# Optimization experiments

Hardware: AMD Instinct MI355X
Metric: run time of the kernel (lower is better)

## Reference

```python
import jax, jax.numpy as jnp
import numpy as np

N, E = 50000, 800000
IN, HID, OUT, L = 512, 64, 40, 16
ALPHA, LAMBDA = 0.1, 0.5


def setup_inputs() -> dict:
    key = jax.random.key(0)
    ks = jax.random.split(key, 8)
    features = jax.random.normal(ks[0], (N, IN), jnp.float32)
    src = jax.random.randint(ks[1], (E,), 0, N)
    dst = jax.random.randint(ks[2], (E,), 0, N)
    # fcs[0]: Linear(IN, HID); fcs[1]: Linear(HID, OUT)
    W_in = jax.random.normal(ks[3], (IN, HID), jnp.float32) / np.sqrt(IN)
    b_in = jnp.zeros((HID,), jnp.float32)
    W_out = jax.random.normal(ks[4], (HID, OUT), jnp.float32) / np.sqrt(HID)
    b_out = jnp.zeros((OUT,), jnp.float32)
    # per-layer GCN2Conv weights (project_initial_features=False -> weight1 & weight2) + bias
    W1 = jax.random.normal(ks[5], (L, HID, HID), jnp.float32) / np.sqrt(HID)
    W2 = jax.random.normal(ks[6], (L, HID, HID), jnp.float32) / np.sqrt(HID)
    b = jnp.zeros((L, HID), jnp.float32)
    return dict(features=features, W_in=W_in, b_in=b_in, W1=W1, W2=W2, b=b,
                W_out=W_out, b_out=b_out, src=src, dst=dst)


def reference(features, W_in, b_in, W1, W2, b, W_out, b_out, src, dst):
    ones = jnp.ones((E,), jnp.float32)
    deg_out = jax.ops.segment_sum(ones, src, num_segments=N)
    deg_in = jax.ops.segment_sum(ones, dst, num_segments=N)
    norm_src = jnp.maximum(deg_out, 1.0) ** -0.5  # [N]
    norm_dst = jnp.maximum(deg_in, 1.0) ** -0.5   # [N]
    betas = jnp.log(LAMBDA / jnp.arange(1, L + 1, dtype=jnp.float32) + 1.0)

    # inference: dropout is identity
    h0 = jax.nn.relu(features @ W_in + b_in)  # [N, HID]

    def layer(h, params):
        w1, w2, bias, beta = params
        # symmetric-normalized sparse propagation: D^-1/2 A D^-1/2 h
        hs = h * norm_src[:, None]
        agg = jax.ops.segment_sum(hs[src], dst, num_segments=N) * norm_dst[:, None]
        f = (1.0 - ALPHA) * agg   # smoothed part
        f0 = ALPHA * h0           # initial residual
        rst = (1.0 - beta) * f + beta * (f @ w1)
        rst = rst + (1.0 - beta) * f0 + beta * (f0 @ w2)
        rst = rst + bias
        return jax.nn.relu(rst), None

    h, _ = jax.lax.scan(layer, h0, (W1, W2, b, betas))
    logits = h @ W_out + b_out  # [N, OUT]
    return jax.nn.log_softmax(logits, axis=1)
```

## Files before the change

### kernel.cpp

```cpp
#include <hip/hip_runtime.h>
#include <math.h>

#define NN 50000
#define NE 800000
#define INF 512
#define HID 64
#define OUTF 40
#define NL 16

#define NBLK 256
#define EPB 3125
#define NBUK 196
#define SLEN (NBUK * NBLK)

#define TN 32
#define FP 72

using short8 = __attribute__((ext_vector_type(8))) short;
using f32x4v = __attribute__((ext_vector_type(4))) float;

__device__ __forceinline__ unsigned int f2bf(float f) {
    unsigned int u = __float_as_uint(f);
    return (u + 0x7fffu + ((u >> 16) & 1u)) >> 16;
}
__device__ __forceinline__ float bflo(unsigned int w) { return __uint_as_float(w << 16); }
__device__ __forceinline__ float bfhi(unsigned int w) { return __uint_as_float(w & 0xffff0000u); }
__device__ __forceinline__ float bfs(unsigned short u) { return __uint_as_float(((unsigned)u) << 16); }


__global__ __launch_bounds__(256) void k_cnt(const int* __restrict__ src, const int* __restrict__ dst,
                                             int* __restrict__ cnt2) {
    __shared__ int hD[NBUK];
    __shared__ int hS[NBUK];
    int t = threadIdx.x;
    int blk = blockIdx.x;
    if (t < NBUK) { hD[t] = 0; hS[t] = 0; }
    __syncthreads();
    int s0 = blk * EPB;
    for (int i = t; i < EPB; i += 256) {
        int e = s0 + i;
        atomicAdd(&hD[dst[e] >> 8], 1);
        atomicAdd(&hS[src[e] >> 8], 1);
    }
    __syncthreads();
    if (t < NBUK) {
        cnt2[t * NBLK + blk] = hD[t];
        cnt2[SLEN + t * NBLK + blk] = hS[t];
    }
}

__global__ __launch_bounds__(256) void gscanA(const int* __restrict__ in, int* __restrict__ incl,
                                              int* __restrict__ bsum, int len) {
    __shared__ int lds[256];
    int i = blockIdx.x * 256 + threadIdx.x;
    int v = (i < len) ? in[i] : 0;
    lds[threadIdx.x] = v;
    __syncthreads();
    for (int off = 1; off < 256; off <<= 1) {
        int t = (threadIdx.x >= off) ? lds[threadIdx.x - off] : 0;
        __syncthreads();
        lds[threadIdx.x] += t;
        __syncthreads();
    }
    if (i < len) incl[i] = lds[threadIdx.x];
    if (threadIdx.x == 255) bsum[blockIdx.x] = lds[255];
}

__global__ __launch_bounds__(512) void gscanB(int* __restrict__ bsum, int nb) {
    __shared__ int lds[512];
    int v = (threadIdx.x < nb) ? bsum[threadIdx.x] : 0;
    lds[threadIdx.x] = v;
    __syncthreads();
    for (int off = 1; off < 512; off <<= 1) {
        int t = (threadIdx.x >= off) ? lds[threadIdx.x - off] : 0;
        __syncthreads();
        lds[threadIdx.x] += t;
        __syncthreads();
    }
    if (threadIdx.x < nb) bsum[threadIdx.x] = lds[threadIdx.x] - v;
}

__global__ __launch_bounds__(256) void gscanC(const int* __restrict__ incl, const int* __restrict__ in,
                                              const int* __restrict__ bsum, int* __restrict__ off, int len) {
    int i = blockIdx.x * 256 + threadIdx.x;
    if (i < len) off[i] = incl[i] - in[i] + bsum[i >> 8] - ((i >= SLEN) ? NE : 0);
}

__global__ __launch_bounds__(256) void k_scat(const int* __restrict__ src, const int* __restrict__ dst,
                                              const int* __restrict__ offD, const int* __restrict__ offS,
                                              uint2* __restrict__ edst, int* __restrict__ esrc) {
    __shared__ int cD[NBUK];
    __shared__ int cS[NBUK];
    int t = threadIdx.x;
    int blk = blockIdx.x;
    if (t < NBUK) { cD[t] = 0; cS[t] = 0; }
    __syncthreads();
    int s0 = blk * EPB;
    for (int i = t; i < EPB; i += 256) {
        int e = s0 + i;
        int d = dst[e];
        int s = src[e];
        int bD = d >> 8;
        int r = atomicAdd(&cD[bD], 1);
        uint2 v;
        v.x = (unsigned)d;
        v.y = (unsigned)s;
        edst[offD[bD * NBLK + blk] + r] = v;
        int bS = s >> 8;
        int r2 = atomicAdd(&cS[bS], 1);
        esrc[offS[bS * NBLK + blk] + r2] = s;
    }
}

__global__ __launch_bounds__(256) void k_build(const uint2* __restrict__ edst, const int* __restrict__ esrc,
                                               const int* __restrict__ offD, const int* __restrict__ offS,
                                               float* __restrict__ nd, int* __restrict__ row_start,
                                               int* __restrict__ col, float* __restrict__ ns) {
    __shared__ int cnt[256];
    __shared__ int ex[256];
    __shared__ int cur[256];
    int t = threadIdx.x;
    if (blockIdx.x < NBUK) {
        int b = blockIdx.x;
        int base = offD[b * NBLK];
        int end = (b < NBUK - 1) ? offD[(b + 1) * NBLK] : NE;
        cnt[t] = 0;
        __syncthreads();
        for (int p = base + t; p < end; p += 256) {
            uint2 ed = edst[p];
            atomicAdd(&cnt[ed.x & 255], 1);
        }
        __syncthreads();
        int v = cnt[t];
        ex[t] = v;
        __syncthreads();
        for (int off = 1; off < 256; off <<= 1) {
            int tv = (t >= off) ? ex[t - off] : 0;
            __syncthreads();
            ex[t] += tv;
            __syncthreads();
        }
        int excl = ex[t] - v;
        cur[t] = excl;
        int node = b * 256 + t;
        if (node < NN) {
            nd[node] = 1.0f / sqrtf((float)max(v, 1));
            row_start[node] = base + excl;
        }
        __syncthreads();
        for (int p = base + t; p < end; p += 256) {
            uint2 ed = edst[p];
            int r = atomicAdd(&cur[ed.x & 255], 1);
            col[base + r] = (int)ed.y;
        }
    } else {
        int b = blockIdx.x - NBUK;
        int base = offS[b * NBLK];
        int end = (b < NBUK - 1) ? offS[(b + 1) * NBLK] : NE;
        cnt[t] = 0;
        __syncthreads();
        for (int p = base + t; p < end; p += 256) {
            atomicAdd(&cnt[esrc[p] & 255], 1);
        }
        __syncthreads();
        int node = b * 256 + t;
        if (node < NN) ns[node] = 1.0f / sqrtf((float)max(cnt[t], 1));
    }
}

__global__ __launch_bounds__(256) void k_wpp(const float* __restrict__ W1, const float* __restrict__ W2,
                                             const float* __restrict__ Win,
                                             unsigned short* __restrict__ wc, unsigned short* __restrict__ wf) {
    int o = blockIdx.x * 256 + threadIdx.x;
    const int NWC = NL * 4 * 4 * 64 * 8;
    if (o < NWC) {
        int j = o & 7;
        int ln = (o >> 3) & 63;
        int c = (o >> 9) & 3;
        int s = (o >> 11) & 3;
        int l = o >> 13;
        int colg = c * 16 + (ln & 15);
        int k = (s & 1) * 32 + ((ln >> 4) << 3) + j;
        float beta = logf(0.5f / (float)(l + 1) + 1.0f);
        const float* W = (s < 2) ? W1 : W2;
        wc[o] = (unsigned short)f2bf(beta * W[((size_t)l * 64 + k) * 64 + colg]);
    } else if (o < NWC + 16 * 4 * 64 * 8) {
        int o2 = o - NWC;
        int jj = o2 & 7;
        int l = (o2 >> 3) & 63;
        int c = (o2 >> 9) & 3;
        int s = o2 >> 11;
        int colg = c * 16 + (l & 15);
        int k = s * 32 + ((l >> 4) << 3) + jj;
        wf[o2] = (unsigned short)f2bf(Win[k * HID + colg]);
    }
}

__global__ __launch_bounds__(256) void k_gemm0(const float* __restrict__ feat, const unsigned short* __restrict__ wf,
                                               float* __restrict__ p0, float* __restrict__ p1) {
    __shared__ unsigned int fS[2048];
    int tid = threadIdx.x;
    int lane = tid & 63;
    int wv = tid >> 6;
    int bx = blockIdx.x;
    int w = bx >> 1;
    int kh = bx & 1;
    int nb = w * 64;
    f32x4v acc[4];
#pragma unroll
    for (int c = 0; c < 4; c++) acc[c] = {0.0f, 0.0f, 0.0f, 0.0f};

    int k0 = kh * 256;
    for (int kc = k0; kc < k0 + 256; kc += 64) {
        if (kc != k0) __syncthreads();
        float4 t[4];
#pragma unroll
        for (int j = 0; j < 4; j++) {
            int i = tid + j * 256;
            int nl = i >> 4;
            int k4 = i & 15;
            int n = min(nb + nl, NN - 1);
            t[j] = *(const float4*)(feat + (size_t)n * INF + kc + k4 * 4);
        }
#pragma unroll
        for (int j = 0; j < 4; j++) {
            int i = tid + j * 256;
            int nl = i >> 4;
            int kl = (i & 15) * 4;
            int s = kl >> 5;
            int kk = kl & 31;
            int lslot = (nl & 15) | ((kk >> 3) << 4);
            int dstu = (((s * 4 + (nl >> 4)) * 64 + lslot) << 2) + ((kk & 4) >> 1);
            fS[dstu] = f2bf(t[j].x) | (f2bf(t[j].y) << 16);
            fS[dstu + 1] = f2bf(t[j].z) | (f2bf(t[j].w) << 16);
        }
        __syncthreads();
#pragma unroll
        for (int s = 0; s < 2; ++s) {
            int sg = (kc + s * 32) >> 5;
            short8 af = *(const short8*)&fS[((s * 4 + wv) * 64 + lane) << 2];
            short8 bf[4];
#pragma unroll
            for (int c = 0; c < 4; ++c)
                bf[c] = *(const short8*)(wf + ((size_t)(sg * 4 + c) * 64 + lane) * 8);
#pragma unroll
            for (int c = 0; c < 4; ++c)
                acc[c] = __builtin_amdgcn_mfma_f32_16x16x32_bf16(af, bf[c], acc[c], 0, 0, 0);
        }
    }
    float* p = kh ? p1 : p0;
    int nodeb = nb + (wv << 4) + ((lane >> 4) << 2);
    int colb = lane & 15;
#pragma unroll
    for (int r = 0; r < 4; ++r) {
        int node = nodeb + r;
        if (node < NN) {
            float* pp = p + (size_t)node * HID + colb;
#pragma unroll
            for (int c = 0; c < 4; ++c) pp[c * 16] = acc[c][r];
        }
    }
}

__global__ __launch_bounds__(256) void k_gfin(const float* __restrict__ p0, const float* __restrict__ p1,
                                              const float* __restrict__ bin, const float* __restrict__ ns,
                                              unsigned int* __restrict__ hs, unsigned int* __restrict__ f0b) {
    int i = blockIdx.x * 256 + threadIdx.x;
    if (i >= NN * 16) return;
    int node = i >> 4;
    int q = i & 15;
    float4 a = ((const float4*)p0)[i];
    float4 b = ((const float4*)p1)[i];
    float4 bi = ((const float4*)bin)[q];
    float nsv = ns[node];
    float q0 = fmaxf(a.x + b.x + bi.x, 0.0f);
    float q1 = fmaxf(a.y + b.y + bi.y, 0.0f);
    float q2 = fmaxf(a.z + b.z + bi.z, 0.0f);
    float q3 = fmaxf(a.w + b.w + bi.w, 0.0f);
    uint2 pk;
    pk.x = f2bf(q0 * nsv) | (f2bf(q1 * nsv) << 16);
    pk.y = f2bf(q2 * nsv) | (f2bf(q3 * nsv) << 16);
    *(uint2*)(hs + (size_t)node * 32 + q * 2) = pk;
    uint2 pf;
    pf.x = f2bf(q0 * 0.1f) | (f2bf(q1 * 0.1f) << 16);
    pf.y = f2bf(q2 * 0.1f) | (f2bf(q3 * 0.1f) << 16);
    *(uint2*)(f0b + (size_t)node * 32 + q * 2) = pf;
}

__global__ __launch_bounds__(256) void k_layer(const unsigned int* __restrict__ hs_in, const int* __restrict__ col,
                                               const int* __restrict__ row_start,
                                               const float* __restrict__ nd, const unsigned int* __restrict__ f0b,
                                               const unsigned short* __restrict__ wc, const float* __restrict__ bias,
                                               const float* __restrict__ ns, float omb,
                                               float* __restrict__ h, unsigned int* __restrict__ hs_out, int write_h) {
    __shared__ unsigned short fS[TN * FP];
    __shared__ unsigned short f0S[TN * FP];
    __shared__ unsigned short oS[TN * FP];
    __shared__ float nsS[TN];
    int tid = threadIdx.x;
    int lane = tid & 63;
    int wv = tid >> 6;
    int nb = blockIdx.x * TN;
    int g = lane >> 4;
    int ql = lane & 15;
    int half = ql >> 3;
    int qb = ql & 7;

    {
        int nl = tid >> 3, sg = tid & 7;
        int n = min(nb + nl, NN - 1);
        uint4 v = *(const uint4*)(f0b + (size_t)n * 32 + sg * 4);
        *(uint4*)&f0S[nl * FP + sg * 8] = v;
    }
    if (tid < TN) nsS[tid] = ns[min(nb + tid, NN - 1)];

    int nlP[2], baseP[2], degP[2], idxP[2];
    float ndP[2];
#pragma unroll
    for (int p = 0; p < 2; ++p) {
        int nl = p * 16 + wv * 4 + g;
        int n = min(nb + nl, NN - 1);
        nlP[p] = nl;
        int base = row_start[n];
        int nxt = (n < NN - 1) ? row_start[n + 1] : NE;
        baseP[p] = base;
        degP[p] = nxt - base;
        ndP[p] = nd[n];
    }
#pragma unroll
    for (int p = 0; p < 2; ++p) {
        idxP[p] = (ql < min(16, degP[p])) ? col[baseP[p] + ql] : 0;
    }

#pragma unroll
    for (int pass = 0; pass < 2; ++pass) {
        int base = baseP[pass];
        int deg = degP[pass];
        int idxv = idxP[pass];
        float a0 = 0.f, a1 = 0.f, a2 = 0.f, a3 = 0.f, a4 = 0.f, a5 = 0.f, a6 = 0.f, a7 = 0.f;
        for (int done = 0; done < deg; done += 16) {
            int cnt = min(16, deg - done);
            int nxt = done + 16;
            int idxn = 0;
            if (nxt < deg && ql < deg - nxt) idxn = col[base + nxt + ql];
            uint4 pv[8];
#pragma unroll
            for (int e = 0; e < 8; ++e) {
                int ec = 2 * e + half;
                int s = __shfl(idxv, (g << 4) | ec, 64);
                uint4 v = {0u, 0u, 0u, 0u};
                if (ec < cnt) v = *(const uint4*)(hs_in + (size_t)s * 32 + qb * 4);
                pv[e] = v;
            }
#pragma unroll
            for (int e = 0; e < 8; ++e) {
                a0 += bflo(pv[e].x); a1 += bfhi(pv[e].x);
                a2 += bflo(pv[e].y); a3 += bfhi(pv[e].y);
                a4 += bflo(pv[e].z); a5 += bfhi(pv[e].z);
                a6 += bflo(pv[e].w); a7 += bfhi(pv[e].w);
            }
            idxv = idxn;
        }
        a0 += __shfl_xor(a0, 8, 64);
        a1 += __shfl_xor(a1, 8, 64);
        a2 += __shfl_xor(a2, 8, 64);
        a3 += __shfl_xor(a3, 8, 64);
        a4 += __shfl_xor(a4, 8, 64);
        a5 += __shfl_xor(a5, 8, 64);
        a6 += __shfl_xor(a6, 8, 64);
        a7 += __shfl_xor(a7, 8, 64);
        float sc = 0.9f * ndP[pass];
        int nl = nlP[pass];
        if (half == 0) {
            uint4 w;
            w.x = f2bf(a0 * sc) | (f2bf(a1 * sc) << 16);
            w.y = f2bf(a2 * sc) | (f2bf(a3 * sc) << 16);
            w.z = f2bf(a4 * sc) | (f2bf(a5 * sc) << 16);
            w.w = f2bf(a6 * sc) | (f2bf(a7 * sc) << 16);
            *(uint4*)&fS[nl * FP + qb * 8] = w;
        }
    }
    __syncthreads();

    int hi = lane >> 4;
    int lo = lane & 15;
    f32x4v acc0 = {0.0f, 0.0f, 0.0f, 0.0f};
    f32x4v acc1 = {0.0f, 0.0f, 0.0f, 0.0f};
#pragma unroll
    for (int s = 0; s < 4; ++s) {
        short8 bf = *(const short8*)(wc + ((size_t)(s * 4 + wv) * 64 + lane) * 8);
        const unsigned short* ab = (s < 2) ? fS : f0S;
        int ko = (s & 1) * 32;
        short8 a0 = *(const short8*)&ab[(0 * 16 + lo) * FP + ko + hi * 8];
        short8 a1 = *(const short8*)&ab[(1 * 16 + lo) * FP + ko + hi * 8];
        acc0 = __builtin_amdgcn_mfma_f32_16x16x32_bf16(a0, bf, acc0, 0, 0, 0);
        acc1 = __builtin_amdgcn_mfma_f32_16x16x32_bf16(a1, bf, acc1, 0, 0, 0);
    }

    int colg = wv * 16 + lo;
    float bv = bias[colg];
#pragma unroll
    for (int m = 0; m < 2; ++m) {
        f32x4v a = m ? acc1 : acc0;
#pragma unroll
        for (int r = 0; r < 4; ++r) {
            int rowl = m * 16 + hi * 4 + r;
            float fv = bfs(fS[rowl * FP + colg]);
            float f0v = bfs(f0S[rowl * FP + colg]);
            float q = fmaxf(a[r] + omb * (fv + f0v) + bv, 0.0f);
            oS[rowl * FP + colg] = (unsigned short)f2bf(q * nsS[rowl]);
            if (write_h) {
                int node = nb + rowl;
                if (node < NN) h[(size_t)node * HID + colg] = q;
            }
        }
    }
    __syncthreads();

    {
        int nl = tid >> 3, sg = tid & 7;
        int node = nb + nl;
        if (node < NN) {
            uint4 v = *(const uint4*)&oS[nl * FP + sg * 8];
            *(uint4*)(hs_out + (size_t)node * 32 + sg * 4) = v;
        }
    }
}

__global__ __launch_bounds__(256) void k_out(const float* __restrict__ h, const float* __restrict__ Wout,
                                             const float* __restrict__ bout, float* __restrict__ out) {
    __shared__ float red_mx[4][64];
    __shared__ float red_s[4][64];
    int tid = threadIdx.x;
    int lane = tid & 63;
    int wv = tid >> 6;
    int half = wv & 1;
    int grp = wv >> 1;
    int node = blockIdx.x * 128 + grp * 64 + lane;
    int nodec = min(node, NN - 1);
    float acc[20];
#pragma unroll
    for (int c = 0; c < 20; c++) acc[c] = 0.0f;
    const float4* hr = (const float4*)(h + (size_t)nodec * HID);
    const float* wb = Wout + half * 20;
    for (int kk = 0; kk < HID / 4; ++kk) {
        float4 a = hr[kk];
        float av[4] = {a.x, a.y, a.z, a.w};
#pragma unroll
        for (int j = 0; j < 4; j++) {
            const float* wr = wb + (size_t)(kk * 4 + j) * OUTF;
#pragma unroll
            for (int c = 0; c < 20; c++) acc[c] += av[j] * wr[c];
        }
    }
    const float* bp = bout + half * 20;
#pragma unroll
    for (int c = 0; c < 20; c++) acc[c] += bp[c];
    float mx = acc[0];
#pragma unroll
    for (int c = 1; c < 20; c++) mx = fmaxf(mx, acc[c]);
    red_mx[wv][lane] = mx;
    __syncthreads();
    float gmx = fmaxf(mx, red_mx[wv ^ 1][lane]);
    float s = 0.0f;
#pragma unroll
    for (int c = 0; c < 20; c++) s += expf(acc[c] - gmx);
    red_s[wv][lane] = s;
    __syncthreads();
    float lse = logf(s + red_s[wv ^ 1][lane]) + gmx;
    if (node < NN) {
        float4* op = (float4*)(out + (size_t)node * OUTF + half * 20);
#pragma unroll
        for (int q = 0; q < 5; q++) {
            float4 v;
            v.x = acc[q * 4 + 0] - lse;
            v.y = acc[q * 4 + 1] - lse;
            v.z = acc[q * 4 + 2] - lse;
            v.w = acc[q * 4 + 3] - lse;
            op[q] = v;
        }
    }
}

extern "C" void kernel_launch(void* const* d_in, const int* in_sizes, int n_in,
                              void* d_out, int out_size, void* d_ws, size_t ws_size,
                              hipStream_t stream) {
    const float* feat = (const float*)d_in[0];
    const float* Win  = (const float*)d_in[1];
    const float* bin  = (const float*)d_in[2];
    const float* W1   = (const float*)d_in[3];
    const float* W2   = (const float*)d_in[4];
    const float* bvec = (const float*)d_in[5];
    const float* Wout = (const float*)d_in[6];
    const float* bout = (const float*)d_in[7];
    const int*   src  = (const int*)d_in[8];
    const int*   dst  = (const int*)d_in[9];
    float* out = (float*)d_out;

    char* ws = (char*)d_ws;
    size_t off = 0;
    auto take = [&](size_t bytes) {
        void* p = ws + off;
        off += (bytes + 255) & ~(size_t)255;
        return p;
    };
    int* bsum      = (int*)take(512 * 4);
    int* row_start = (int*)take(NN * 4);
    int* col       = (int*)take(NE * 4);
    float* nsrc    = (float*)take(NN * 4);
    float* ndst    = (float*)take(NN * 4);
    int* cnt2      = (int*)take(2 * SLEN * 4);
    int* off2      = (int*)take(2 * SLEN * 4);
    int* sincl     = (int*)take(2 * SLEN * 4);
    unsigned short* wcat  = (unsigned short*)take((size_t)NL * 4 * 4 * 64 * 8 * 2);
    unsigned short* wfrag = (unsigned short*)take((size_t)INF * HID * 2);
    unsigned int* f0b = (unsigned int*)take((size_t)NN * HID * 2);
    float* hbuf    = (float*)take((size_t)NN * HID * 4);
    float* part1   = (float*)take((size_t)NN * HID * 4);
    unsigned int* hsA = (unsigned int*)take((size_t)NN * HID * 2);
    unsigned int* hsB = (unsigned int*)take((size_t)NN * HID * 2);

    uint2* edst = (uint2*)hbuf;
    int* esrc   = (int*)part1;
    int* offD = off2;
    int* offS = off2 + SLEN;

    const int NB_W = (NN + 63) / 64;
    const int NB_L = (NN + TN - 1) / TN;
    const int NB_O = (NN + 127) / 128;
    const int NB_S2 = 2 * SLEN / 256;

    k_cnt<<<NBLK, 256, 0, stream>>>(src, dst, cnt2);
    gscanA<<<NB_S2, 256, 0, stream>>>(cnt2, sincl, bsum, 2 * SLEN);
    gscanB<<<1, 512, 0, stream>>>(bsum, NB_S2);
    gscanC<<<NB_S2, 256, 0, stream>>>(sincl, cnt2, bsum, off2, 2 * SLEN);
    k_scat<<<NBLK, 256, 0, stream>>>(src, dst, offD, offS, edst, esrc);
    k_build<<<2 * NBUK, 256, 0, stream>>>(edst, esrc, offD, offS, ndst, row_start, col, nsrc);

    k_wpp<<<(NL * 4 * 4 * 64 * 8 + INF * HID + 255) / 256, 256, 0, stream>>>(W1, W2, Win, wcat, wfrag);
    k_gemm0<<<2 * NB_W, 256, 0, stream>>>(feat, wfrag, hbuf, part1);
    k_gfin<<<(NN * 16 + 255) / 256, 256, 0, stream>>>(hbuf, part1, bin, nsrc, hsA, f0b);

    for (int l = 0; l < NL; ++l) {
        const unsigned int* hin = (l & 1) ? hsB : hsA;
        unsigned int* hout = (l & 1) ? hsA : hsB;
        float beta = logf(0.5f / (float)(l + 1) + 1.0f);
        float omb = 1.0f - beta;
        k_layer<<<NB_L, 256, 0, stream>>>(hin, col, row_start, ndst, f0b,
                                          wcat + (size_t)l * 4 * 4 * 64 * 8, bvec + l * HID,
                                          nsrc, omb, hbuf, hout, (l == NL - 1) ? 1 : 0);
    }
    k_out<<<NB_O, 256, 0, stream>>>(hbuf, Wout, bout, out);
}
```

Before: 547.0 us.

## Halve per-layer tile to 16 nodes per block for more blocks

Shrinks the propagation/GEMM kernel tile from 32 to 16 nodes per block, so each wave aggregates one node instead of two and each block issues one MFMA chain instead of two. This doubles the grid (50000/16 divides evenly, so the bounds clamps are dropped) and aims for more parallelism and latency hiding in the gather. In exchange, per-block fixed costs such as weight-fragment loads and barriers are paid twice as often, and the two independent gather passes per wave that overlapped memory latency are lost.

```diff
diff --git a/kernel.cpp b/kernel.cpp
--- a/kernel.cpp
+++ b/kernel.cpp
@@ -13,7 +13,7 @@
 #define NBUK 196
 #define SLEN (NBUK * NBLK)
 
-#define TN 32
+#define TN 16
 #define FP 72
 
 using short8 = __attribute__((ext_vector_type(8))) short;
@@ -306,37 +306,23 @@
     int half = ql >> 3;
     int qb = ql & 7;
 
-    {
+    if (tid < TN * 8) {
         int nl = tid >> 3, sg = tid & 7;
-        int n = min(nb + nl, NN - 1);
+        int n = nb + nl;
         uint4 v = *(const uint4*)(f0b + (size_t)n * 32 + sg * 4);
         *(uint4*)&f0S[nl * FP + sg * 8] = v;
     }
-    if (tid < TN) nsS[tid] = ns[min(nb + tid, NN - 1)];
-
-    int nlP[2], baseP[2], degP[2], idxP[2];
-    float ndP[2];
-#pragma unroll
-    for (int p = 0; p < 2; ++p) {
-        int nl = p * 16 + wv * 4 + g;
-        int n = min(nb + nl, NN - 1);
-        nlP[p] = nl;
-        int base = row_start[n];
-        int nxt = (n < NN - 1) ? row_start[n + 1] : NE;
-        baseP[p] = base;
-        degP[p] = nxt - base;
-        ndP[p] = nd[n];
-    }
-#pragma unroll
-    for (int p = 0; p < 2; ++p) {
-        idxP[p] = (ql < min(16, degP[p])) ? col[baseP[p] + ql] : 0;
-    }
-
-#pragma unroll
-    for (int pass = 0; pass < 2; ++pass) {
-        int base = baseP[pass];
-        int deg = degP[pass];
-        int idxv = idxP[pass];
+    if (tid < TN) nsS[tid] = ns[nb + tid];
+
+    int nl = wv * 4 + g;
+    int n = nb + nl;
+    int base = row_start[n];
+    int nxt0 = (n < NN - 1) ? row_start[n + 1] : NE;
+    int deg = nxt0 - base;
+    float ndv = nd[n];
+    int idxv = (ql < min(16, deg)) ? col[base + ql] : 0;
+
+    {
         float a0 = 0.f, a1 = 0.f, a2 = 0.f, a3 = 0.f, a4 = 0.f, a5 = 0.f, a6 = 0.f, a7 = 0.f;
         for (int done = 0; done < deg; done += 16) {
             int cnt = min(16, deg - done);
@@ -369,8 +355,7 @@
         a5 += __shfl_xor(a5, 8, 64);
         a6 += __shfl_xor(a6, 8, 64);
         a7 += __shfl_xor(a7, 8, 64);
-        float sc = 0.9f * ndP[pass];
-        int nl = nlP[pass];
+        float sc = 0.9f * ndv;
         if (half == 0) {
             uint4 w;
             w.x = f2bf(a0 * sc) | (f2bf(a1 * sc) << 16);
@@ -385,45 +370,34 @@
     int hi = lane >> 4;
     int lo = lane & 15;
     f32x4v acc0 = {0.0f, 0.0f, 0.0f, 0.0f};
-    f32x4v acc1 = {0.0f, 0.0f, 0.0f, 0.0f};
 #pragma unroll
     for (int s = 0; s < 4; ++s) {
         short8 bf = *(const short8*)(wc + ((size_t)(s * 4 + wv) * 64 + lane) * 8);
         const unsigned short* ab = (s < 2) ? fS : f0S;
         int ko = (s & 1) * 32;
-        short8 a0 = *(const short8*)&ab[(0 * 16 + lo) * FP + ko + hi * 8];
-        short8 a1 = *(const short8*)&ab[(1 * 16 + lo) * FP + ko + hi * 8];
+        short8 a0 = *(const short8*)&ab[lo * FP + ko + hi * 8];
         acc0 = __builtin_amdgcn_mfma_f32_16x16x32_bf16(a0, bf, acc0, 0, 0, 0);
-        acc1 = __builtin_amdgcn_mfma_f32_16x16x32_bf16(a1, bf, acc1, 0, 0, 0);
     }
 
     int colg = wv * 16 + lo;
     float bv = bias[colg];
 #pragma unroll
-    for (int m = 0; m < 2; ++m) {
-        f32x4v a = m ? acc1 : acc0;
-#pragma unroll
-        for (int r = 0; r < 4; ++r) {
-            int rowl = m * 16 + hi * 4 + r;
-            float fv = bfs(fS[rowl * FP + colg]);
-            float f0v = bfs(f0S[rowl * FP + colg]);
-            float q = fmaxf(a[r] + omb * (fv + f0v) + bv, 0.0f);
-            oS[rowl * FP + colg] = (unsigned short)f2bf(q * nsS[rowl]);
-            if (write_h) {
-                int node = nb + rowl;
-                if (node < NN) h[(size_t)node * HID + colg] = q;
-            }
-        }
-    }
-    __syncthreads();
-
-    {
-        int nl = tid >> 3, sg = tid & 7;
-        int node = nb + nl;
-        if (node < NN) {
-            uint4 v = *(const uint4*)&oS[nl * FP + sg * 8];
-            *(uint4*)(hs_out + (size_t)node * 32 + sg * 4) = v;
-        }
+    for (int r = 0; r < 4; ++r) {
+        int rowl = hi * 4 + r;
+        float fv = bfs(fS[rowl * FP + colg]);
+        float f0v = bfs(f0S[rowl * FP + colg]);
+        float q = fmaxf(acc0[r] + omb * (fv + f0v) + bv, 0.0f);
+        oS[rowl * FP + colg] = (unsigned short)f2bf(q * nsS[rowl]);
+        if (write_h) {
+            h[(size_t)(nb + rowl) * HID + colg] = q;
+        }
+    }
+    __syncthreads();
+
+    if (tid < TN * 8) {
+        int nl2 = tid >> 3, sg = tid & 7;
+        uint4 v = *(const uint4*)&oS[nl2 * FP + sg * 8];
+        *(uint4*)(hs_out + (size_t)(nb + nl2) * 32 + sg * 4) = v;
     }
 }
 
```

Result: no change. 541.5 us (-1.0%).
